# Kernel tuning notes

Measured on AMD Instinct MI355X. Metric: run time of the kernel, lower is better.

## Reference

```python
import jax, jax.numpy as jnp
import numpy as np

B, S, D, H = 1, 4096, 512, 8
HD = D // H  # head_dims = 64


def setup_inputs() -> dict:
    key = jax.random.key(0)
    ks = jax.random.split(key, 12)
    scale = 0.02
    query = jax.random.normal(ks[0], (B, S, D), dtype=jnp.float32)
    key_t = jax.random.normal(ks[1], (B, S, D), dtype=jnp.float32)
    value = jax.random.normal(ks[2], (B, S, D), dtype=jnp.float32)
    mask = jax.random.randint(ks[3], (B, 1, S, S), 0, 2, dtype=jnp.int32)
    # per-head projection params (torch Linear: y = x @ W.T + b)
    Wq = jax.random.normal(ks[4], (HD, HD), dtype=jnp.float32) * scale
    bq = jax.random.normal(ks[5], (HD,), dtype=jnp.float32) * scale
    Wk = jax.random.normal(ks[6], (HD, HD), dtype=jnp.float32) * scale
    bk = jax.random.normal(ks[7], (HD,), dtype=jnp.float32) * scale
    Wv = jax.random.normal(ks[8], (HD, HD), dtype=jnp.float32) * scale
    bv = jax.random.normal(ks[9], (HD,), dtype=jnp.float32) * scale
    Wfc = jax.random.normal(ks[10], (D, D), dtype=jnp.float32) * scale
    bfc = jax.random.normal(ks[11], (D,), dtype=jnp.float32) * scale
    return {"query": query, "key": key_t, "value": value, "mask": mask,
            "Wq": Wq, "bq": bq, "Wk": Wk, "bk": bk, "Wv": Wv, "bv": bv,
            "Wfc": Wfc, "bfc": bfc}


def reference(query, key, value, mask, Wq, bq, Wk, bk, Wv, bv, Wfc, bfc):
    Batch, q_len, _ = query.shape
    k_len = key.shape[1]
    # reshape to [b, s, h, d] then apply per-head linear projections
    q = query.reshape(Batch, q_len, H, HD) @ Wq.T + bq
    k = key.reshape(Batch, k_len, H, HD) @ Wk.T + bk
    v = value.reshape(Batch, k_len, H, HD) @ Wv.T + bv
    # raw scores [b, h, q, k]; mask applied BEFORE scaling (as in original)
    score = jnp.einsum('bqhd,bkhd->bhqk', q, k)
    score = jnp.where(mask == 0, jnp.float32(-1e20), score)
    attn = jax.nn.softmax(score / jnp.sqrt(jnp.float32(HD)), axis=-1)
    out = jnp.einsum('bhqv,bvhd->bqhd', attn, v).reshape(Batch, q_len, D)
    return out @ Wfc.T + bfc
```

## Files before the change

### kernel.cpp

```cpp
#include <hip/hip_runtime.h>
#include <hip/hip_bf16.h>

#define S_LEN 4096
#define DMODEL 512
#define NHEAD 8
#define HDIM 64

typedef __bf16 bf16x8 __attribute__((ext_vector_type(8)));
typedef __bf16 bf16x4 __attribute__((ext_vector_type(4)));
typedef float f32x4 __attribute__((ext_vector_type(4)));

__device__ __forceinline__ void gload_lds16(const void* g, void* l) {
    __builtin_amdgcn_global_load_lds((const __attribute__((address_space(1))) void*)g,
                                     (__attribute__((address_space(3))) void*)l, 16, 0, 0);
}

__global__ __launch_bounds__(256) void proj_qk_kernel(const float* __restrict__ xq,
                                                      const float* __restrict__ xk,
                                                      const float* __restrict__ Wq,
                                                      const float* __restrict__ bq,
                                                      const float* __restrict__ Wk,
                                                      const float* __restrict__ bk,
                                                      __bf16* __restrict__ yq,
                                                      __bf16* __restrict__ yk) {
    int t = threadIdx.x, wave = t >> 6, lane = t & 63, lg = lane >> 4, lc = lane & 15;
    int r0 = blockIdx.x * 64 + wave * 16;
    const float* xrq = xq + (size_t)(r0 + lc) * 64 + lg * 8;
    const float* xrk = xk + (size_t)(r0 + lc) * 64 + lg * 8;
    bf16x8 aq[2], ak[2];
#pragma unroll
    for (int c = 0; c < 2; ++c) {
        f32x4 u0 = *(const f32x4*)(xrq + c * 32);
        f32x4 u1 = *(const f32x4*)(xrq + c * 32 + 4);
        f32x4 v0 = *(const f32x4*)(xrk + c * 32);
        f32x4 v1 = *(const f32x4*)(xrk + c * 32 + 4);
        bf16x8 a, b;
#pragma unroll
        for (int j = 0; j < 4; ++j) {
            a[j] = (__bf16)u0[j]; a[4 + j] = (__bf16)u1[j];
            b[j] = (__bf16)v0[j]; b[4 + j] = (__bf16)v1[j];
        }
        aq[c] = a; ak[c] = b;
    }
#pragma unroll
    for (int nt = 0; nt < 4; ++nt) {
        const float* wq = Wq + (size_t)(nt * 16 + lc) * 64 + lg * 8;
        const float* wk = Wk + (size_t)(nt * 16 + lc) * 64 + lg * 8;
        f32x4 cq = {0, 0, 0, 0}, ck = {0, 0, 0, 0};
#pragma unroll
        for (int c = 0; c < 2; ++c) {
            f32x4 u0 = *(const f32x4*)(wq + c * 32);
            f32x4 u1 = *(const f32x4*)(wq + c * 32 + 4);
            f32x4 v0 = *(const f32x4*)(wk + c * 32);
            f32x4 v1 = *(const f32x4*)(wk + c * 32 + 4);
            bf16x8 bw, bw2;
#pragma unroll
            for (int j = 0; j < 4; ++j) {
                bw[j] = (__bf16)u0[j]; bw[4 + j] = (__bf16)u1[j];
                bw2[j] = (__bf16)v0[j]; bw2[4 + j] = (__bf16)v1[j];
            }
            cq = __builtin_amdgcn_mfma_f32_16x16x32_bf16(aq[c], bw, cq, 0, 0, 0);
            ck = __builtin_amdgcn_mfma_f32_16x16x32_bf16(ak[c], bw2, ck, 0, 0, 0);
        }
        float bqv = bq[nt * 16 + lc], bkv = bk[nt * 16 + lc];
#pragma unroll
        for (int r = 0; r < 4; ++r) {
            yq[(size_t)(r0 + lg * 4 + r) * 64 + nt * 16 + lc] = (__bf16)(cq[r] + bqv);
            yk[(size_t)(r0 + lg * 4 + r) * 64 + nt * 16 + lc] = (__bf16)(ck[r] + bkv);
        }
    }
}

__global__ __launch_bounds__(256) void proj_v_kernel(const float* __restrict__ x,
                                                     const float* __restrict__ W,
                                                     const float* __restrict__ b,
                                                     __bf16* __restrict__ vt) {
    __shared__ float T[64][65];
    int h = blockIdx.x & 7, s0 = (blockIdx.x >> 3) * 64;
    int t = threadIdx.x, wave = t >> 6, lane = t & 63, lg = lane >> 4, lc = lane & 15;
    const float* xr = x + ((size_t)(s0 + wave * 16 + lc) * 8 + h) * 64 + lg * 8;
    bf16x8 av[2];
#pragma unroll
    for (int c = 0; c < 2; ++c) {
        f32x4 u0 = *(const f32x4*)(xr + c * 32);
        f32x4 u1 = *(const f32x4*)(xr + c * 32 + 4);
        bf16x8 a;
#pragma unroll
        for (int j = 0; j < 4; ++j) { a[j] = (__bf16)u0[j]; a[4 + j] = (__bf16)u1[j]; }
        av[c] = a;
    }
#pragma unroll
    for (int nt = 0; nt < 4; ++nt) {
        const float* wv = W + (size_t)(nt * 16 + lc) * 64 + lg * 8;
        f32x4 cv = {0, 0, 0, 0};
#pragma unroll
        for (int c = 0; c < 2; ++c) {
            f32x4 u0 = *(const f32x4*)(wv + c * 32);
            f32x4 u1 = *(const f32x4*)(wv + c * 32 + 4);
            bf16x8 bw;
#pragma unroll
            for (int j = 0; j < 4; ++j) { bw[j] = (__bf16)u0[j]; bw[4 + j] = (__bf16)u1[j]; }
            cv = __builtin_amdgcn_mfma_f32_16x16x32_bf16(av[c], bw, cv, 0, 0, 0);
        }
        float bvv = b[nt * 16 + lc];
#pragma unroll
        for (int r = 0; r < 4; ++r) T[wave * 16 + lg * 4 + r][nt * 16 + lc] = cv[r] + bvv;
    }
    __syncthreads();
    int d = t >> 2, qr = t & 3;
    bf16x8 w0, w1;
#pragma unroll
    for (int i = 0; i < 8; ++i) {
        w0[i] = (__bf16)T[qr * 16 + i][d];
        w1[i] = (__bf16)T[qr * 16 + 8 + i][d];
    }
    __bf16* dst = vt + ((size_t)h * 64 + d) * 4096 + s0 + qr * 16;
    *(bf16x8*)(dst) = w0;
    *(bf16x8*)(dst + 8) = w1;
}

__global__ __launch_bounds__(256) void maskpack_kernel(const int* __restrict__ mask,
                                                       unsigned int* __restrict__ pack) {
    int t = threadIdx.x, lane = t & 63;
    int wid = blockIdx.x * 4 + (t >> 6);
#pragma unroll 4
    for (int it = 0; it < 32; ++it) {
        int gw = wid * 32 + it;
        int qi = gw >> 6, seg = gw & 63;
        unsigned long long bits = __ballot(mask[(size_t)qi * 4096 + seg * 64 + lane] != 0);
        if (lane == 0)
            *(unsigned long long*)(&pack[(size_t)qi * 128 + seg * 2]) = bits;
    }
}

__global__ __launch_bounds__(256) void cvt_kernel(const float* __restrict__ src,
                                                  __bf16* __restrict__ dst, int n) {
    int i = blockIdx.x * 256 + threadIdx.x;
    if (i < n) dst[i] = (__bf16)src[i];
}

__global__ __launch_bounds__(256, 4) void attn_kernel(const __bf16* __restrict__ qb,
                                                      const __bf16* __restrict__ kb,
                                                      const __bf16* __restrict__ vt,
                                                      const unsigned int* __restrict__ mp,
                                                      int kv_len,
                                                      float* __restrict__ opart,
                                                      float* __restrict__ stats,
                                                      __bf16* __restrict__ ao) {
    int bid = blockIdx.x;
    int h = bid & 7, qt = (bid >> 3) & 63, sp = bid >> 9;
    int kv0 = sp * kv_len;
    int t = threadIdx.x, wave = t >> 6, lane = t & 63, lg = lane >> 4, lc = lane & 15;
    int q0 = qt * 64 + wave * 16;

    __shared__ __bf16 Kt[2][64 * 64];
    __shared__ __bf16 Vt[2][64 * 64];
    __shared__ __bf16 P[4][16 * 64];

    int srow = lane >> 3;
    int cg = (lane & 7) ^ srow;

    const __bf16* qrow = qb + ((size_t)(q0 + lc) * 8 + h) * 64 + lg * 8;
    bf16x8 qf0 = *(const bf16x8*)(qrow);
    bf16x8 qf1 = *(const bf16x8*)(qrow + 32);

    f32x4 o0 = {0,0,0,0}, o1 = {0,0,0,0}, o2 = {0,0,0,0}, o3 = {0,0,0,0};
    float m_ = -3e38f, l_ = 0.f;

    const unsigned int* mrow = mp + (size_t)(q0 + lc) * 128;
    const __bf16* vbase = vt + (size_t)h * 64 * 4096;

#pragma unroll
    for (int j = wave * 2; j < wave * 2 + 2; ++j) {
        gload_lds16(kb + (size_t)(kv0 + j * 8 + srow) * 512 + h * 64 + cg * 8, &Kt[0][j * 512]);
        gload_lds16(vbase + (size_t)(j * 8 + srow) * 4096 + kv0 + cg * 8,      &Vt[0][j * 512]);
    }
    __syncthreads();

    int nsteps = kv_len >> 6;
    for (int step = 0; step < nsteps; ++step) {
        int cur = step & 1;
        int kb_i = kv0 + step * 64;
        if (step < nsteps - 1) {
            int nxt = kb_i + 64;
#pragma unroll
            for (int j = wave * 2; j < wave * 2 + 2; ++j) {
                gload_lds16(kb + (size_t)(nxt + j * 8 + srow) * 512 + h * 64 + cg * 8, &Kt[cur ^ 1][j * 512]);
                gload_lds16(vbase + (size_t)(j * 8 + srow) * 4096 + nxt + cg * 8,      &Vt[cur ^ 1][j * 512]);
            }
        }
        const char* Kb = (const char*)&Kt[cur][0];
        f32x4 sc[4];
#pragma unroll
        for (int kc = 0; kc < 4; ++kc) {
            int row = kc * 16 + lc;
            int sw = (row & 7) << 4;
            bf16x8 kf0 = *(const bf16x8*)(Kb + ((row * 128 + lg * 16) ^ sw));
            bf16x8 kf1 = *(const bf16x8*)(Kb + ((row * 128 + 64 + lg * 16) ^ sw));
            f32x4 z = {0,0,0,0};
            z = __builtin_amdgcn_mfma_f32_16x16x32_bf16(kf0, qf0, z, 0, 0, 0);
            z = __builtin_amdgcn_mfma_f32_16x16x32_bf16(kf1, qf1, z, 0, 0, 0);
            sc[kc] = z;
        }
        unsigned int w0 = mrow[kb_i >> 5], w1 = mrow[(kb_i >> 5) + 1];
        float vals[4][4];
        float vmax = -3e38f;
#pragma unroll
        for (int kc = 0; kc < 4; ++kc) {
            unsigned int wsel = (kc < 2) ? w0 : w1;
#pragma unroll
            for (int r = 0; r < 4; ++r) {
                int bitpos = (kc & 1) * 16 + lg * 4 + r;
                float val = ((wsel >> bitpos) & 1u) ? sc[kc][r] * 0.125f : -1.25e19f;
                vals[kc][r] = val;
                vmax = fmaxf(vmax, val);
            }
        }
        vmax = fmaxf(vmax, __shfl_xor(vmax, 16));
        vmax = fmaxf(vmax, __shfl_xor(vmax, 32));
        if (__any(vmax > m_ + 8.0f)) {
            float mn = fmaxf(m_, vmax);
            float corr = __expf(m_ - mn);
            m_ = mn;
            l_ *= corr;
            f32x4 cv;
#pragma unroll
            for (int r = 0; r < 4; ++r) cv[r] = __shfl(corr, lg * 4 + r);
            o0 *= cv; o1 *= cv; o2 *= cv; o3 *= cv;
        }
        float ps = 0.f;
#pragma unroll
        for (int kc = 0; kc < 4; ++kc)
#pragma unroll
            for (int r = 0; r < 4; ++r) {
                float p = __expf(vals[kc][r] - m_);
                vals[kc][r] = p;
                ps += p;
            }
        ps += __shfl_xor(ps, 16);
        ps += __shfl_xor(ps, 32);
        l_ += ps;
        char* pbase = (char*)&P[wave][0];
#pragma unroll
        for (int kc = 0; kc < 4; ++kc) {
            bf16x4 pk;
#pragma unroll
            for (int r = 0; r < 4; ++r) pk[r] = (__bf16)vals[kc][r];
            int byte = (lc * 128 + kc * 32 + lg * 8) ^ ((lc & 7) << 4);
            *(bf16x4*)(pbase + byte) = pk;
        }
        const char* Vb = (const char*)&Vt[cur][0];
        int swv = (lc & 7) << 4;
#pragma unroll
        for (int kk = 0; kk < 2; ++kk) {
            int pbyte = ((lc * 64 + kk * 32 + lg * 8) * 2) ^ swv;
            bf16x8 pf = *(const bf16x8*)((const char*)&P[wave][0] + pbyte);
            int ch = (kk * 4 + lg) * 16;
            o0 = __builtin_amdgcn_mfma_f32_16x16x32_bf16(pf, *(const bf16x8*)(Vb + (((0 * 16 + lc) * 128 + ch) ^ swv)), o0, 0, 0, 0);
            o1 = __builtin_amdgcn_mfma_f32_16x16x32_bf16(pf, *(const bf16x8*)(Vb + (((1 * 16 + lc) * 128 + ch) ^ swv)), o1, 0, 0, 0);
            o2 = __builtin_amdgcn_mfma_f32_16x16x32_bf16(pf, *(const bf16x8*)(Vb + (((2 * 16 + lc) * 128 + ch) ^ swv)), o2, 0, 0, 0);
            o3 = __builtin_amdgcn_mfma_f32_16x16x32_bf16(pf, *(const bf16x8*)(Vb + (((3 * 16 + lc) * 128 + ch) ^ swv)), o3, 0, 0, 0);
        }
        __syncthreads();
    }
    if (opart) {
        if (lg == 0) {
            size_t rh = (size_t)sp * 32768 + (size_t)(q0 + lc) * 8 + h;
            stats[rh * 2]     = m_;
            stats[rh * 2 + 1] = l_;
        }
#pragma unroll
        for (int r = 0; r < 4; ++r) {
            size_t rh = (size_t)sp * 32768 + (size_t)(q0 + lg * 4 + r) * 8 + h;
            float* dst = opart + rh * 64;
            dst[0 * 16 + lc] = o0[r];
            dst[1 * 16 + lc] = o1[r];
            dst[2 * 16 + lc] = o2[r];
            dst[3 * 16 + lc] = o3[r];
        }
    } else {
        float linv = 1.0f / l_;
#pragma unroll
        for (int r = 0; r < 4; ++r) {
            float inv = __shfl(linv, lg * 4 + r);
            int row = q0 + lg * 4 + r;
            __bf16* dst = ao + (size_t)row * 512 + h * 64;
            dst[0 * 16 + lc] = (__bf16)(o0[r] * inv);
            dst[1 * 16 + lc] = (__bf16)(o1[r] * inv);
            dst[2 * 16 + lc] = (__bf16)(o2[r] * inv);
            dst[3 * 16 + lc] = (__bf16)(o3[r] * inv);
        }
    }
}

__global__ __launch_bounds__(256) void combine_kernel(const float* __restrict__ opart,
                                                      const float* __restrict__ stats,
                                                      __bf16* __restrict__ ao, int nsplit) {
    int t = threadIdx.x, lane = t & 63, w = t >> 6;
    int rh = blockIdx.x * 4 + w;
    float m_i[4], l_i[4];
    float M = -3e38f;
#pragma unroll 4
    for (int sp = 0; sp < nsplit; ++sp) {
        m_i[sp] = stats[((size_t)sp * 32768 + rh) * 2];
        l_i[sp] = stats[((size_t)sp * 32768 + rh) * 2 + 1];
        M = fmaxf(M, m_i[sp]);
    }
    float L = 0.f, acc = 0.f;
#pragma unroll 4
    for (int sp = 0; sp < nsplit; ++sp) {
        float scl = __expf(m_i[sp] - M);
        L += l_i[sp] * scl;
        acc += opart[((size_t)sp * 32768 + rh) * 64 + lane] * scl;
    }
    int row = rh >> 3, h = rh & 7;
    ao[(size_t)row * 512 + h * 64 + lane] = (__bf16)(acc / L);
}

__global__ __launch_bounds__(256) void fc_kernel(const __bf16* __restrict__ ao,
                                                 const __bf16* __restrict__ Wb,
                                                 const float* __restrict__ bfc,
                                                 float* __restrict__ out) {
    int bid = blockIdx.x;
    int stile = bid >> 3, nt = bid & 7;
    int t = threadIdx.x, wave = t >> 6, lane = t & 63, lg = lane >> 4, lc = lane & 15;
    int s0 = stile * 64 + wave * 16;
    int n0 = nt * 64;
    f32x4 c0 = {0,0,0,0}, c1 = {0,0,0,0}, c2 = {0,0,0,0}, c3 = {0,0,0,0};
    for (int k0 = 0; k0 < 512; k0 += 32) {
        bf16x8 af = *(const bf16x8*)(ao + (size_t)(s0 + lc) * 512 + k0 + lg * 8);
        const __bf16* wb = Wb + k0 + lg * 8;
        c0 = __builtin_amdgcn_mfma_f32_16x16x32_bf16(af, *(const bf16x8*)(wb + (size_t)(n0 + 0 * 16 + lc) * 512), c0, 0, 0, 0);
        c1 = __builtin_amdgcn_mfma_f32_16x16x32_bf16(af, *(const bf16x8*)(wb + (size_t)(n0 + 1 * 16 + lc) * 512), c1, 0, 0, 0);
        c2 = __builtin_amdgcn_mfma_f32_16x16x32_bf16(af, *(const bf16x8*)(wb + (size_t)(n0 + 2 * 16 + lc) * 512), c2, 0, 0, 0);
        c3 = __builtin_amdgcn_mfma_f32_16x16x32_bf16(af, *(const bf16x8*)(wb + (size_t)(n0 + 3 * 16 + lc) * 512), c3, 0, 0, 0);
    }
#pragma unroll
    for (int r = 0; r < 4; ++r) {
        int row = s0 + lg * 4 + r;
        float* dst = out + (size_t)row * 512 + n0;
        dst[0 * 16 + lc] = c0[r] + bfc[n0 + 0 * 16 + lc];
        dst[1 * 16 + lc] = c1[r] + bfc[n0 + 1 * 16 + lc];
        dst[2 * 16 + lc] = c2[r] + bfc[n0 + 2 * 16 + lc];
        dst[3 * 16 + lc] = c3[r] + bfc[n0 + 3 * 16 + lc];
    }
}

extern "C" void kernel_launch(void* const* d_in, const int* in_sizes, int n_in,
                              void* d_out, int out_size, void* d_ws, size_t ws_size,
                              hipStream_t stream) {
    const float* query = (const float*)d_in[0];
    const float* key   = (const float*)d_in[1];
    const float* value = (const float*)d_in[2];
    const int*   mask  = (const int*)d_in[3];
    const float* Wq  = (const float*)d_in[4];
    const float* bq  = (const float*)d_in[5];
    const float* Wk  = (const float*)d_in[6];
    const float* bk  = (const float*)d_in[7];
    const float* Wv  = (const float*)d_in[8];
    const float* bv  = (const float*)d_in[9];
    const float* Wfc = (const float*)d_in[10];
    const float* bfc = (const float*)d_in[11];

    char* ws = (char*)d_ws;
    const size_t MB = 1024 * 1024;
    __bf16* q_bf   = (__bf16*)(ws + 0 * MB);
    __bf16* k_bf   = (__bf16*)(ws + 4 * MB);
    __bf16* vt     = (__bf16*)(ws + 8 * MB);
    __bf16* ao     = (__bf16*)(ws + 12 * MB);
    __bf16* wfc_bf = (__bf16*)(ws + 16 * MB);
    unsigned int* mpack = (unsigned int*)(ws + 17 * MB);
    const size_t base = 19 * MB;
    int nsplit = (ws_size >= base + 2 * (8 * MB) + 524288) ? 2 : 1;
    float* opart = (float*)(ws + base);
    float* stats = (float*)(ws + base + (size_t)nsplit * 8 * MB);

    proj_qk_kernel<<<512, 256, 0, stream>>>(query, key, Wq, bq, Wk, bk, q_bf, k_bf);
    proj_v_kernel<<<512, 256, 0, stream>>>(value, Wv, bv, vt);
    maskpack_kernel<<<2048, 256, 0, stream>>>(mask, mpack);
    cvt_kernel<<<1024, 256, 0, stream>>>(Wfc, wfc_bf, 262144);
    if (nsplit > 1) {
        attn_kernel<<<512 * nsplit, 256, 0, stream>>>(q_bf, k_bf, vt, mpack,
                                                      S_LEN / nsplit, opart, stats, ao);
        combine_kernel<<<8192, 256, 0, stream>>>(opart, stats, ao, nsplit);
    } else {
        attn_kernel<<<512, 256, 0, stream>>>(q_bf, k_bf, vt, mpack,
                                             S_LEN, nullptr, nullptr, ao);
    }
    fc_kernel<<<512, 256, 0, stream>>>(ao, wfc_bf, bfc, (float*)d_out);
}
```

Baseline: 140.0 us.

## Drop online softmax max tracking, compute row sums via MFMA, merge prep kernels

Result: faster. 124.2 us (-11.3%).

```diff
diff --git a/kernel.cpp b/kernel.cpp
--- a/kernel.cpp
+++ b/kernel.cpp
@@ -10,133 +10,149 @@
 typedef __bf16 bf16x4 __attribute__((ext_vector_type(4)));
 typedef float f32x4 __attribute__((ext_vector_type(4)));
 
+#define S2EXP 0.18033688011112042f
+
 __device__ __forceinline__ void gload_lds16(const void* g, void* l) {
     __builtin_amdgcn_global_load_lds((const __attribute__((address_space(1))) void*)g,
                                      (__attribute__((address_space(3))) void*)l, 16, 0, 0);
 }
 
-__global__ __launch_bounds__(256) void proj_qk_kernel(const float* __restrict__ xq,
-                                                      const float* __restrict__ xk,
-                                                      const float* __restrict__ Wq,
-                                                      const float* __restrict__ bq,
-                                                      const float* __restrict__ Wk,
-                                                      const float* __restrict__ bk,
-                                                      __bf16* __restrict__ yq,
-                                                      __bf16* __restrict__ yk) {
+__global__ __launch_bounds__(256) void proj_all_kernel(const float* __restrict__ xq,
+                                                       const float* __restrict__ xk,
+                                                       const float* __restrict__ xv,
+                                                       const float* __restrict__ Wq,
+                                                       const float* __restrict__ bq,
+                                                       const float* __restrict__ Wk,
+                                                       const float* __restrict__ bk,
+                                                       const float* __restrict__ Wv,
+                                                       const float* __restrict__ bv,
+                                                       __bf16* __restrict__ yq,
+                                                       __bf16* __restrict__ yk,
+                                                       __bf16* __restrict__ vt) {
+    __shared__ float T[64][65];
+    int bid = blockIdx.x;
     int t = threadIdx.x, wave = t >> 6, lane = t & 63, lg = lane >> 4, lc = lane & 15;
-    int r0 = blockIdx.x * 64 + wave * 16;
-    const float* xrq = xq + (size_t)(r0 + lc) * 64 + lg * 8;
-    const float* xrk = xk + (size_t)(r0 + lc) * 64 + lg * 8;
-    bf16x8 aq[2], ak[2];
-#pragma unroll
-    for (int c = 0; c < 2; ++c) {
-        f32x4 u0 = *(const f32x4*)(xrq + c * 32);
-        f32x4 u1 = *(const f32x4*)(xrq + c * 32 + 4);
-        f32x4 v0 = *(const f32x4*)(xrk + c * 32);
-        f32x4 v1 = *(const f32x4*)(xrk + c * 32 + 4);
-        bf16x8 a, b;
-#pragma unroll
-        for (int j = 0; j < 4; ++j) {
-            a[j] = (__bf16)u0[j]; a[4 + j] = (__bf16)u1[j];
-            b[j] = (__bf16)v0[j]; b[4 + j] = (__bf16)v1[j];
-        }
-        aq[c] = a; ak[c] = b;
-    }
-#pragma unroll
-    for (int nt = 0; nt < 4; ++nt) {
-        const float* wq = Wq + (size_t)(nt * 16 + lc) * 64 + lg * 8;
-        const float* wk = Wk + (size_t)(nt * 16 + lc) * 64 + lg * 8;
-        f32x4 cq = {0, 0, 0, 0}, ck = {0, 0, 0, 0};
+    if (bid < 512) {
+        int r0 = bid * 64 + wave * 16;
+        const float* xrq = xq + (size_t)(r0 + lc) * 64 + lg * 8;
+        const float* xrk = xk + (size_t)(r0 + lc) * 64 + lg * 8;
+        bf16x8 aq[2], ak[2];
 #pragma unroll
         for (int c = 0; c < 2; ++c) {
-            f32x4 u0 = *(const f32x4*)(wq + c * 32);
-            f32x4 u1 = *(const f32x4*)(wq + c * 32 + 4);
-            f32x4 v0 = *(const f32x4*)(wk + c * 32);
-            f32x4 v1 = *(const f32x4*)(wk + c * 32 + 4);
-            bf16x8 bw, bw2;
+            f32x4 u0 = *(const f32x4*)(xrq + c * 32);
+            f32x4 u1 = *(const f32x4*)(xrq + c * 32 + 4);
+            f32x4 v0 = *(const f32x4*)(xrk + c * 32);
+            f32x4 v1 = *(const f32x4*)(xrk + c * 32 + 4);
+            bf16x8 a, b;
 #pragma unroll
             for (int j = 0; j < 4; ++j) {
-                bw[j] = (__bf16)u0[j]; bw[4 + j] = (__bf16)u1[j];
-                bw2[j] = (__bf16)v0[j]; bw2[4 + j] = (__bf16)v1[j];
-            }
-            cq = __builtin_amdgcn_mfma_f32_16x16x32_bf16(aq[c], bw, cq, 0, 0, 0);
-            ck = __builtin_amdgcn_mfma_f32_16x16x32_bf16(ak[c], bw2, ck, 0, 0, 0);
-        }
-        float bqv = bq[nt * 16 + lc], bkv = bk[nt * 16 + lc];
-#pragma unroll
-        for (int r = 0; r < 4; ++r) {
-            yq[(size_t)(r0 + lg * 4 + r) * 64 + nt * 16 + lc] = (__bf16)(cq[r] + bqv);
-            yk[(size_t)(r0 + lg * 4 + r) * 64 + nt * 16 + lc] = (__bf16)(ck[r] + bkv);
-        }
-    }
-}
-
-__global__ __launch_bounds__(256) void proj_v_kernel(const float* __restrict__ x,
-                                                     const float* __restrict__ W,
-                                                     const float* __restrict__ b,
-                                                     __bf16* __restrict__ vt) {
-    __shared__ float T[64][65];
-    int h = blockIdx.x & 7, s0 = (blockIdx.x >> 3) * 64;
-    int t = threadIdx.x, wave = t >> 6, lane = t & 63, lg = lane >> 4, lc = lane & 15;
-    const float* xr = x + ((size_t)(s0 + wave * 16 + lc) * 8 + h) * 64 + lg * 8;
-    bf16x8 av[2];
-#pragma unroll
-    for (int c = 0; c < 2; ++c) {
-        f32x4 u0 = *(const f32x4*)(xr + c * 32);
-        f32x4 u1 = *(const f32x4*)(xr + c * 32 + 4);
-        bf16x8 a;
-#pragma unroll
-        for (int j = 0; j < 4; ++j) { a[j] = (__bf16)u0[j]; a[4 + j] = (__bf16)u1[j]; }
-        av[c] = a;
-    }
-#pragma unroll
-    for (int nt = 0; nt < 4; ++nt) {
-        const float* wv = W + (size_t)(nt * 16 + lc) * 64 + lg * 8;
-        f32x4 cv = {0, 0, 0, 0};
+                a[j] = (__bf16)u0[j]; a[4 + j] = (__bf16)u1[j];
+                b[j] = (__bf16)v0[j]; b[4 + j] = (__bf16)v1[j];
+            }
+            aq[c] = a; ak[c] = b;
+        }
+#pragma unroll
+        for (int nt = 0; nt < 4; ++nt) {
+            const float* wq = Wq + (size_t)(nt * 16 + lc) * 64 + lg * 8;
+            const float* wk = Wk + (size_t)(nt * 16 + lc) * 64 + lg * 8;
+            f32x4 cq = {0, 0, 0, 0}, ck = {0, 0, 0, 0};
+#pragma unroll
+            for (int c = 0; c < 2; ++c) {
+                f32x4 u0 = *(const f32x4*)(wq + c * 32);
+                f32x4 u1 = *(const f32x4*)(wq + c * 32 + 4);
+                f32x4 v0 = *(const f32x4*)(wk + c * 32);
+                f32x4 v1 = *(const f32x4*)(wk + c * 32 + 4);
+                bf16x8 bw, bw2;
+#pragma unroll
+                for (int j = 0; j < 4; ++j) {
+                    bw[j] = (__bf16)u0[j]; bw[4 + j] = (__bf16)u1[j];
+                    bw2[j] = (__bf16)v0[j]; bw2[4 + j] = (__bf16)v1[j];
+                }
+                cq = __builtin_amdgcn_mfma_f32_16x16x32_bf16(aq[c], bw, cq, 0, 0, 0);
+                ck = __builtin_amdgcn_mfma_f32_16x16x32_bf16(ak[c], bw2, ck, 0, 0, 0);
+            }
+            float bqv = bq[nt * 16 + lc], bkv = bk[nt * 16 + lc];
+#pragma unroll
+            for (int r = 0; r < 4; ++r) {
+                yq[(size_t)(r0 + lg * 4 + r) * 64 + nt * 16 + lc] = (__bf16)(cq[r] + bqv);
+                yk[(size_t)(r0 + lg * 4 + r) * 64 + nt * 16 + lc] = (__bf16)(ck[r] + bkv);
+            }
+        }
+    } else {
+        int vb = bid - 512;
+        int h = vb & 7, s0 = (vb >> 3) * 64;
+        const float* xr = xv + ((size_t)(s0 + wave * 16 + lc) * 8 + h) * 64 + lg * 8;
+        bf16x8 av[2];
 #pragma unroll
         for (int c = 0; c < 2; ++c) {
-            f32x4 u0 = *(const f32x4*)(wv + c * 32);
-            f32x4 u1 = *(const f32x4*)(wv + c * 32 + 4);
-            bf16x8 bw;
-#pragma unroll
-            for (int j = 0; j < 4; ++j) { bw[j] = (__bf16)u0[j]; bw[4 + j] = (__bf16)u1[j]; }
-            cv = __builtin_amdgcn_mfma_f32_16x16x32_bf16(av[c], bw, cv, 0, 0, 0);
-        }
-        float bvv = b[nt * 16 + lc];
-#pragma unroll
-        for (int r = 0; r < 4; ++r) T[wave * 16 + lg * 4 + r][nt * 16 + lc] = cv[r] + bvv;
-    }
-    __syncthreads();
-    int d = t >> 2, qr = t & 3;
-    bf16x8 w0, w1;
-#pragma unroll
-    for (int i = 0; i < 8; ++i) {
-        w0[i] = (__bf16)T[qr * 16 + i][d];
-        w1[i] = (__bf16)T[qr * 16 + 8 + i][d];
-    }
-    __bf16* dst = vt + ((size_t)h * 64 + d) * 4096 + s0 + qr * 16;
-    *(bf16x8*)(dst) = w0;
-    *(bf16x8*)(dst + 8) = w1;
-}
-
-__global__ __launch_bounds__(256) void maskpack_kernel(const int* __restrict__ mask,
-                                                       unsigned int* __restrict__ pack) {
-    int t = threadIdx.x, lane = t & 63;
-    int wid = blockIdx.x * 4 + (t >> 6);
+            f32x4 u0 = *(const f32x4*)(xr + c * 32);
+            f32x4 u1 = *(const f32x4*)(xr + c * 32 + 4);
+            bf16x8 a;
+#pragma unroll
+            for (int j = 0; j < 4; ++j) { a[j] = (__bf16)u0[j]; a[4 + j] = (__bf16)u1[j]; }
+            av[c] = a;
+        }
+#pragma unroll
+        for (int nt = 0; nt < 4; ++nt) {
+            const float* wv = Wv + (size_t)(nt * 16 + lc) * 64 + lg * 8;
+            f32x4 cv = {0, 0, 0, 0};
+#pragma unroll
+            for (int c = 0; c < 2; ++c) {
+                f32x4 u0 = *(const f32x4*)(wv + c * 32);
+                f32x4 u1 = *(const f32x4*)(wv + c * 32 + 4);
+                bf16x8 bw;
+#pragma unroll
+                for (int j = 0; j < 4; ++j) { bw[j] = (__bf16)u0[j]; bw[4 + j] = (__bf16)u1[j]; }
+                cv = __builtin_amdgcn_mfma_f32_16x16x32_bf16(av[c], bw, cv, 0, 0, 0);
+            }
+            float bvv = bv[nt * 16 + lc];
+#pragma unroll
+            for (int r = 0; r < 4; ++r) T[wave * 16 + lg * 4 + r][nt * 16 + lc] = cv[r] + bvv;
+        }
+        __syncthreads();
+        int d = t >> 2, qr = t & 3;
+        bf16x8 w0, w1;
+#pragma unroll
+        for (int i = 0; i < 8; ++i) {
+            w0[i] = (__bf16)T[qr * 16 + i][d];
+            w1[i] = (__bf16)T[qr * 16 + 8 + i][d];
+        }
+        __bf16* dst = vt + ((size_t)h * 64 + d) * 4096 + s0 + qr * 16;
+        *(bf16x8*)(dst) = w0;
+        *(bf16x8*)(dst + 8) = w1;
+    }
+}
+
+__global__ __launch_bounds__(256) void prep_kernel(const int* __restrict__ mask,
+                                                   unsigned int* __restrict__ pack,
+                                                   const float* __restrict__ Wfc,
+                                                   __bf16* __restrict__ wfc_bf) {
+    int bid = blockIdx.x;
+    int t = threadIdx.x;
+    if (bid < 2048) {
+        int lane = t & 63;
+        int wid = bid * 4 + (t >> 6);
 #pragma unroll 4
-    for (int it = 0; it < 32; ++it) {
-        int gw = wid * 32 + it;
-        int qi = gw >> 6, seg = gw & 63;
-        unsigned long long bits = __ballot(mask[(size_t)qi * 4096 + seg * 64 + lane] != 0);
-        if (lane == 0)
-            *(unsigned long long*)(&pack[(size_t)qi * 128 + seg * 2]) = bits;
-    }
-}
-
-__global__ __launch_bounds__(256) void cvt_kernel(const float* __restrict__ src,
-                                                  __bf16* __restrict__ dst, int n) {
-    int i = blockIdx.x * 256 + threadIdx.x;
-    if (i < n) dst[i] = (__bf16)src[i];
+        for (int it = 0; it < 32; ++it) {
+            int gw = wid * 32 + it;
+            int qi = gw >> 6, seg = gw & 63;
+            unsigned long long bits = __ballot(mask[(size_t)qi * 4096 + seg * 64 + lane] != 0);
+            if (lane == 0)
+                *(unsigned long long*)(&pack[(size_t)qi * 128 + seg * 2]) = bits;
+        }
+    } else {
+        int b = bid - 2048;
+        const f32x4* s4 = (const f32x4*)Wfc;
+#pragma unroll
+        for (int i = 0; i < 8; ++i) {
+            int idx = (b * 8 + i) * 256 + t;
+            f32x4 v = s4[idx];
+            bf16x4 o;
+#pragma unroll
+            for (int j = 0; j < 4; ++j) o[j] = (__bf16)v[j];
+            *(bf16x4*)(wfc_bf + (size_t)idx * 4) = o;
+        }
+    }
 }
 
 __global__ __launch_bounds__(256, 4) void attn_kernel(const __bf16* __restrict__ qb,
@@ -164,8 +180,12 @@
     bf16x8 qf0 = *(const bf16x8*)(qrow);
     bf16x8 qf1 = *(const bf16x8*)(qrow + 32);
 
+    bf16x8 onesf;
+#pragma unroll
+    for (int j = 0; j < 8; ++j) onesf[j] = (__bf16)1.0f;
+
     f32x4 o0 = {0,0,0,0}, o1 = {0,0,0,0}, o2 = {0,0,0,0}, o3 = {0,0,0,0};
-    float m_ = -3e38f, l_ = 0.f;
+    f32x4 l_acc = {0,0,0,0};
 
     const unsigned int* mrow = mp + (size_t)(q0 + lc) * 128;
     const __bf16* vbase = vt + (size_t)h * 64 * 4096;
@@ -202,50 +222,19 @@
             z = __builtin_amdgcn_mfma_f32_16x16x32_bf16(kf1, qf1, z, 0, 0, 0);
             sc[kc] = z;
         }
-        unsigned int w0 = mrow[kb_i >> 5], w1 = mrow[(kb_i >> 5) + 1];
-        float vals[4][4];
-        float vmax = -3e38f;
+        uint2 mw = *(const uint2*)(mrow + (kb_i >> 5));
+        char* pbase = (char*)&P[wave][0];
 #pragma unroll
         for (int kc = 0; kc < 4; ++kc) {
-            unsigned int wsel = (kc < 2) ? w0 : w1;
+            unsigned int wsel = (kc < 2) ? mw.x : mw.y;
+            bf16x4 pk;
 #pragma unroll
             for (int r = 0; r < 4; ++r) {
                 int bitpos = (kc & 1) * 16 + lg * 4 + r;
-                float val = ((wsel >> bitpos) & 1u) ? sc[kc][r] * 0.125f : -1.25e19f;
-                vals[kc][r] = val;
-                vmax = fmaxf(vmax, val);
-            }
-        }
-        vmax = fmaxf(vmax, __shfl_xor(vmax, 16));
-        vmax = fmaxf(vmax, __shfl_xor(vmax, 32));
-        if (__any(vmax > m_ + 8.0f)) {
-            float mn = fmaxf(m_, vmax);
-            float corr = __expf(m_ - mn);
-            m_ = mn;
-            l_ *= corr;
-            f32x4 cv;
-#pragma unroll
-            for (int r = 0; r < 4; ++r) cv[r] = __shfl(corr, lg * 4 + r);
-            o0 *= cv; o1 *= cv; o2 *= cv; o3 *= cv;
-        }
-        float ps = 0.f;
-#pragma unroll
-        for (int kc = 0; kc < 4; ++kc)
-#pragma unroll
-            for (int r = 0; r < 4; ++r) {
-                float p = __expf(vals[kc][r] - m_);
-                vals[kc][r] = p;
-                ps += p;
-            }
-        ps += __shfl_xor(ps, 16);
-        ps += __shfl_xor(ps, 32);
-        l_ += ps;
-        char* pbase = (char*)&P[wave][0];
-#pragma unroll
-        for (int kc = 0; kc < 4; ++kc) {
-            bf16x4 pk;
-#pragma unroll
-            for (int r = 0; r < 4; ++r) pk[r] = (__bf16)vals[kc][r];
+                float p = __builtin_amdgcn_exp2f(sc[kc][r] * S2EXP);
+                int sel = ((int)(wsel << (31 - bitpos))) >> 31;
+                pk[r] = (__bf16)__int_as_float(__float_as_int(p) & sel);
+            }
             int byte = (lc * 128 + kc * 32 + lg * 8) ^ ((lc & 7) << 4);
             *(bf16x4*)(pbase + byte) = pk;
         }
@@ -253,8 +242,9 @@
         int swv = (lc & 7) << 4;
 #pragma unroll
         for (int kk = 0; kk < 2; ++kk) {
-            int pbyte = ((lc * 64 + kk * 32 + lg * 8) * 2) ^ swv;
+            int pbyte = (lc * 128 + kk * 64 + lg * 16) ^ swv;
             bf16x8 pf = *(const bf16x8*)((const char*)&P[wave][0] + pbyte);
+            l_acc = __builtin_amdgcn_mfma_f32_16x16x32_bf16(pf, onesf, l_acc, 0, 0, 0);
             int ch = (kk * 4 + lg) * 16;
             o0 = __builtin_amdgcn_mfma_f32_16x16x32_bf16(pf, *(const bf16x8*)(Vb + (((0 * 16 + lc) * 128 + ch) ^ swv)), o0, 0, 0, 0);
             o1 = __builtin_amdgcn_mfma_f32_16x16x32_bf16(pf, *(const bf16x8*)(Vb + (((1 * 16 + lc) * 128 + ch) ^ swv)), o1, 0, 0, 0);
@@ -264,10 +254,10 @@
         __syncthreads();
     }
     if (opart) {
-        if (lg == 0) {
-            size_t rh = (size_t)sp * 32768 + (size_t)(q0 + lc) * 8 + h;
-            stats[rh * 2]     = m_;
-            stats[rh * 2 + 1] = l_;
+        if (lc == 0) {
+#pragma unroll
+            for (int r = 0; r < 4; ++r)
+                stats[(size_t)sp * 32768 + (size_t)(q0 + lg * 4 + r) * 8 + h] = l_acc[r];
         }
 #pragma unroll
         for (int r = 0; r < 4; ++r) {
@@ -279,10 +269,9 @@
             dst[3 * 16 + lc] = o3[r];
         }
     } else {
-        float linv = 1.0f / l_;
 #pragma unroll
         for (int r = 0; r < 4; ++r) {
-            float inv = __shfl(linv, lg * 4 + r);
+            float inv = 1.0f / l_acc[r];
             int row = q0 + lg * 4 + r;
             __bf16* dst = ao + (size_t)row * 512 + h * 64;
             dst[0 * 16 + lc] = (__bf16)(o0[r] * inv);
@@ -295,24 +284,11 @@
 
 __global__ __launch_bounds__(256) void combine_kernel(const float* __restrict__ opart,
                                                       const float* __restrict__ stats,
-                                                      __bf16* __restrict__ ao, int nsplit) {
+                                                      __bf16* __restrict__ ao) {
     int t = threadIdx.x, lane = t & 63, w = t >> 6;
     int rh = blockIdx.x * 4 + w;
-    float m_i[4], l_i[4];
-    float M = -3e38f;
-#pragma unroll 4
-    for (int sp = 0; sp < nsplit; ++sp) {
-        m_i[sp] = stats[((size_t)sp * 32768 + rh) * 2];
-        l_i[sp] = stats[((size_t)sp * 32768 + rh) * 2 + 1];
-        M = fmaxf(M, m_i[sp]);
-    }
-    float L = 0.f, acc = 0.f;
-#pragma unroll 4
-    for (int sp = 0; sp < nsplit; ++sp) {
-        float scl = __expf(m_i[sp] - M);
-        L += l_i[sp] * scl;
-        acc += opart[((size_t)sp * 32768 + rh) * 64 + lane] * scl;
-    }
+    float L = stats[rh] + stats[32768 + rh];
+    float acc = opart[(size_t)rh * 64 + lane] + opart[(size_t)(32768 + rh) * 64 + lane];
     int row = rh >> 3, h = rh & 7;
     ao[(size_t)row * 512 + h * 64 + lane] = (__bf16)(acc / L);
 }
@@ -375,14 +351,13 @@
     float* opart = (float*)(ws + base);
     float* stats = (float*)(ws + base + (size_t)nsplit * 8 * MB);
 
-    proj_qk_kernel<<<512, 256, 0, stream>>>(query, key, Wq, bq, Wk, bk, q_bf, k_bf);
-    proj_v_kernel<<<512, 256, 0, stream>>>(value, Wv, bv, vt);
-    maskpack_kernel<<<2048, 256, 0, stream>>>(mask, mpack);
-    cvt_kernel<<<1024, 256, 0, stream>>>(Wfc, wfc_bf, 262144);
+    proj_all_kernel<<<1024, 256, 0, stream>>>(query, key, value, Wq, bq, Wk, bk, Wv, bv,
+                                              q_bf, k_bf, vt);
+    prep_kernel<<<2080, 256, 0, stream>>>(mask, mpack, Wfc, wfc_bf);
     if (nsplit > 1) {
         attn_kernel<<<512 * nsplit, 256, 0, stream>>>(q_bf, k_bf, vt, mpack,
                                                       S_LEN / nsplit, opart, stats, ao);
-        combine_kernel<<<8192, 256, 0, stream>>>(opart, stats, ao, nsplit);
+        combine_kernel<<<8192, 256, 0, stream>>>(opart, stats, ao);
     } else {
         attn_kernel<<<512, 256, 0, stream>>>(q_bf, k_bf, vt, mpack,
                                              S_LEN, nullptr, nullptr, ao);
```
